# Kernel tuning notes

Hardware: AMD Instinct MI355X
Metric: run time of the kernel (lower is better)

The kernel has to match this reference:

```python
import jax, jax.numpy as jnp
import numpy as np

EMBED = 1024
HEADS = 16
HEAD_DIM = EMBED // HEADS
OUT_DIM = 1024


def setup_inputs() -> dict:
    key = jax.random.key(0)
    ks = jax.random.split(key, 8)
    N, L = 2, 2048
    values = jax.random.normal(ks[0], (N, L, EMBED), dtype=jnp.float32)
    keys_t = jax.random.normal(ks[1], (N, L, EMBED), dtype=jnp.float32)
    query = jax.random.normal(ks[2], (N, L, EMBED), dtype=jnp.float32)
    s = 1.0 / np.sqrt(HEAD_DIM)
    Wv = jax.random.normal(ks[3], (HEAD_DIM, HEAD_DIM), dtype=jnp.float32) * s
    Wk = jax.random.normal(ks[4], (HEAD_DIM, HEAD_DIM), dtype=jnp.float32) * s
    Wq = jax.random.normal(ks[5], (HEAD_DIM, HEAD_DIM), dtype=jnp.float32) * s
    Wout = jax.random.normal(ks[6], (OUT_DIM, EMBED), dtype=jnp.float32) * (1.0 / np.sqrt(EMBED))
    bout = jax.random.normal(ks[7], (OUT_DIM,), dtype=jnp.float32) * 0.01
    return {"values": values, "keys": keys_t, "query": query,
            "Wv": Wv, "Wk": Wk, "Wq": Wq, "Wout": Wout, "bout": bout}


def reference(values, keys, query, Wv, Wk, Wq, Wout, bout):
    N, Lq, _ = query.shape
    Lk = keys.shape[1]
    # split into heads: (N, L, H, D)
    v = values.reshape(N, Lk, HEADS, HEAD_DIM)
    k = keys.reshape(N, Lk, HEADS, HEAD_DIM)
    q = query.reshape(N, Lq, HEADS, HEAD_DIM)
    # per-head shared linear projections (torch Linear: x @ W.T, no bias)
    v = jnp.einsum('nlhd,ed->nlhe', v, Wv)
    k = jnp.einsum('nlhd,ed->nlhe', k, Wk)
    q = jnp.einsum('nqhd,ed->nqhe', q, Wq)
    # scores (N, H, Q, K); NOTE: scale is 1/sqrt(embed_size), per original code
    scores = jnp.einsum('nqhd,nkhd->nhqk', q, k) / jnp.sqrt(jnp.float32(EMBED))
    attn = jax.nn.softmax(scores, axis=-1)
    out = jnp.einsum('nhqk,nkhd->nqhd', attn, v).reshape(N, Lq, EMBED)
    # fc_out: x @ Wout.T + bout
    return out @ Wout.T + bout
```

## Files before the change

kernel.cpp:

```cpp
#include <hip/hip_runtime.h>
#include <cstdint>

typedef __attribute__((ext_vector_type(8))) short short8;
typedef __attribute__((ext_vector_type(4))) float floatx4;
typedef __attribute__((ext_vector_type(4))) _Float16 half4;

#define DEV __device__ __forceinline__

constexpr int NB = 2, Lseq = 2048, NH = 16, HD = 64, EMB = 1024;
constexpr float QSCALE = 0.03125f * 1.4426950408889634f;

DEV uint16_t f2bf(float f) {
  uint32_t x = __builtin_bit_cast(uint32_t, f);
  x += 0x7fffu + ((x >> 16) & 1u);
  return (uint16_t)(x >> 16);
}

DEV uint32_t pack2(float lo, float hi) {
  uint32_t a = __builtin_bit_cast(uint32_t, lo) + 0x8000u;
  uint32_t b = __builtin_bit_cast(uint32_t, hi) + 0x8000u;
  return __builtin_amdgcn_perm(b, a, 0x07060302);
}

DEV uint32_t packh2(float lo, float hi) {
  return __builtin_bit_cast(uint32_t, __builtin_amdgcn_cvt_pkrtz(lo, hi));
}

DEV void gl_lds16(const void* g, void* l) {
  __builtin_amdgcn_global_load_lds((const __attribute__((address_space(1))) void*)g,
                                   (__attribute__((address_space(3))) void*)l, 16, 0, 0);
}

DEV short8 ld8bf(const float* p, float sc) {
  float4 u = *(const float4*)p;
  float4 v = *(const float4*)(p + 4);
  union { short8 s; uint32_t d[4]; } r;
  r.d[0] = pack2(u.x * sc, u.y * sc);
  r.d[1] = pack2(u.z * sc, u.w * sc);
  r.d[2] = pack2(v.x * sc, v.y * sc);
  r.d[3] = pack2(v.z * sc, v.w * sc);
  return r.s;
}

__global__ __launch_bounds__(256) void prep_kernel(
    const float* __restrict__ values, const float* __restrict__ keysrc,
    const float* __restrict__ query, const float* __restrict__ Wv,
    const float* __restrict__ Wk, const float* __restrict__ Wq,
    const float* __restrict__ Wout,
    uint16_t* __restrict__ qp, uint16_t* __restrict__ kp,
    uint16_t* __restrict__ vp, uint16_t* __restrict__ wbf) {
  const int t = threadIdx.x, w = t >> 6, lane = t & 63;
  const int quad = lane >> 4, l16 = lane & 15;
  const int wid = blockIdx.x * 4 + w;
  const int mat = wid >> 10, sub = wid & 1023;

  if (mat == 3) {
#pragma unroll
    for (int i = 0; i < 4; ++i) {
      int idx = sub * 256 + i * 64 + lane;
      float4 v = ((const float4*)Wout)[idx];
      uint2 p;
      p.x = pack2(v.x, v.y);
      p.y = pack2(v.z, v.w);
      ((uint2*)wbf)[idx] = p;
    }
    return;
  }

  floatx4 c[4][4];
#pragma unroll
  for (int i = 0; i < 4; ++i)
#pragma unroll
    for (int j = 0; j < 4; ++j) c[i][j] = floatx4{0.f, 0.f, 0.f, 0.f};

  if (mat < 2) {
    const float* src = mat ? keysrc : query;
    const float* W   = mat ? Wk : Wq;
    const float asc  = mat ? 1.f : QSCALE;
    uint16_t* dst    = mat ? kp : qp;
    const int R0 = sub * 64;
    short8 a[4][2], b[4][2];
#pragma unroll
    for (int dc = 0; dc < 2; ++dc) {
#pragma unroll
      for (int f = 0; f < 4; ++f) {
        a[f][dc] = ld8bf(W + (size_t)(f * 16 + l16) * 64 + dc * 32 + quad * 8, asc);
        b[f][dc] = ld8bf(src + (size_t)(R0 + f * 16 + l16) * 64 + dc * 32 + quad * 8, 1.f);
      }
    }
#pragma unroll
    for (int dc = 0; dc < 2; ++dc)
#pragma unroll
      for (int mf = 0; mf < 4; ++mf)
#pragma unroll
        for (int nf = 0; nf < 4; ++nf)
          c[mf][nf] = __builtin_amdgcn_mfma_f32_16x16x32_bf16(a[mf][dc], b[nf][dc], c[mf][nf], 0, 0, 0);
#pragma unroll
    for (int nf = 0; nf < 4; ++nf) {
      int r = R0 + nf * 16 + l16;
      int h = r & 15, l = (r >> 4) & 2047, n = r >> 15;
      uint16_t* drow = dst + ((size_t)(n * 16 + h) * 2048 + l) * 64;
#pragma unroll
      for (int mf = 0; mf < 4; ++mf) {
        uint2 pk;
        pk.x = pack2(c[mf][nf][0], c[mf][nf][1]);
        pk.y = pack2(c[mf][nf][2], c[mf][nf][3]);
        *(uint2*)(drow + mf * 16 + quad * 4) = pk;
      }
    }
  } else {
    const int nh = sub >> 5, L0 = (sub & 31) * 64;
    const int n = nh >> 4, h = nh & 15;
    short8 a[4][2], b[4][2];
#pragma unroll
    for (int dc = 0; dc < 2; ++dc) {
#pragma unroll
      for (int f = 0; f < 4; ++f) {
        a[f][dc] = ld8bf(values + (size_t)(n * 2048 + L0 + f * 16 + l16) * 1024 + h * 64 + dc * 32 + quad * 8, 1.f);
        b[f][dc] = ld8bf(Wv + (size_t)(f * 16 + l16) * 64 + dc * 32 + quad * 8, 1.f);
      }
    }
#pragma unroll
    for (int dc = 0; dc < 2; ++dc)
#pragma unroll
      for (int mf = 0; mf < 4; ++mf)
#pragma unroll
        for (int nf = 0; nf < 4; ++nf)
          c[mf][nf] = __builtin_amdgcn_mfma_f32_16x16x32_bf16(a[mf][dc], b[nf][dc], c[mf][nf], 0, 0, 0);
#pragma unroll
    for (int nf = 0; nf < 4; ++nf) {
      int d = nf * 16 + l16;
      uint16_t* drow = vp + ((size_t)nh * 64 + d) * 2048 + L0;
#pragma unroll
      for (int mf = 0; mf < 4; ++mf) {
        uint2 pk;
        pk.x = packh2(c[mf][nf][0], c[mf][nf][1]);
        pk.y = packh2(c[mf][nf][2], c[mf][nf][3]);
        *(uint2*)(drow + mf * 16 + quad * 4) = pk;
      }
    }
  }
}

__global__ __launch_bounds__(256, 4) void flash_kernel(const uint16_t* __restrict__ qp,
                                                       const uint16_t* __restrict__ kp,
                                                       const uint16_t* __restrict__ vp,
                                                       float* __restrict__ opart,
                                                       float* __restrict__ psum_g) {
  constexpr int kbn = 16;
  __shared__ uint16_t Kt[2][64 * 64];
  __shared__ uint16_t Vt[2][64 * 64];
  const int t = threadIdx.x;
  const int w = t >> 6, lane = t & 63, quad = lane >> 4, l16 = lane & 15;
  const int nh = blockIdx.x, qt = blockIdx.y, kh = blockIdx.z;
  const int q0 = qt * 128 + w * 32;
  const uint16_t* Qb = qp + (size_t)nh * Lseq * HD;
  const uint16_t* Kb = kp + (size_t)nh * Lseq * HD + (size_t)kh * kbn * 64 * 64;
  const uint16_t* Vb = vp + (size_t)nh * HD * Lseq;
  const int vcol0 = kh * kbn * 64;
  const int srow = lane >> 3, sc8 = (lane & 7) ^ (lane >> 3);

  short8 bq[2][2];
#pragma unroll
  for (int qb = 0; qb < 2; ++qb) {
    bq[qb][0] = *(const short8*)(Qb + (q0 + qb * 16 + l16) * 64 + quad * 8);
    bq[qb][1] = *(const short8*)(Qb + (q0 + qb * 16 + l16) * 64 + 32 + quad * 8);
  }

  floatx4 o[4][2];
  floatx4 lfr[2];
#pragma unroll
  for (int i = 0; i < 4; ++i)
#pragma unroll
    for (int qb = 0; qb < 2; ++qb) o[i][qb] = floatx4{0.f, 0.f, 0.f, 0.f};
  lfr[0] = lfr[1] = floatx4{0.f, 0.f, 0.f, 0.f};
  const _Float16 one = (_Float16)1.0f;
  const half4 vone = {one, one, one, one};

#pragma unroll
  for (int i = 0; i < 2; ++i) {
    int r0 = w * 16 + i * 8;
    gl_lds16(Kb + (r0 + srow) * 64 + sc8 * 8, &Kt[0][r0 * 64]);
    gl_lds16(Vb + (size_t)(r0 + srow) * Lseq + vcol0 + sc8 * 8, &Vt[0][r0 * 64]);
  }

  for (int kb = 0; kb < kbn; ++kb) {
    __syncthreads();
    const int cur = kb & 1;
    if (kb + 1 < kbn) {
      const int nxt = cur ^ 1;
      const uint16_t* kg = Kb + (kb + 1) * (64 * 64);
#pragma unroll
      for (int i = 0; i < 2; ++i) {
        int r0 = w * 16 + i * 8;
        gl_lds16(kg + (r0 + srow) * 64 + sc8 * 8, &Kt[nxt][r0 * 64]);
        gl_lds16(Vb + (size_t)(r0 + srow) * Lseq + vcol0 + (kb + 1) * 64 + sc8 * 8, &Vt[nxt][r0 * 64]);
      }
    }

    floatx4 s[4][2];
#pragma unroll
    for (int kb16 = 0; kb16 < 4; ++kb16)
#pragma unroll
      for (int qb = 0; qb < 2; ++qb) s[kb16][qb] = floatx4{0.f, 0.f, 0.f, 0.f};
#pragma unroll
    for (int dc = 0; dc < 2; ++dc) {
#pragma unroll
      for (int kb16 = 0; kb16 < 4; ++kb16) {
        int row = kb16 * 16 + l16;
        short8 ak = *(const short8*)(&Kt[cur][row * 64 + ((dc * 4 + quad) ^ (row & 7)) * 8]);
        s[kb16][0] = __builtin_amdgcn_mfma_f32_16x16x32_bf16(ak, bq[0][dc], s[kb16][0], 0, 0, 0);
        s[kb16][1] = __builtin_amdgcn_mfma_f32_16x16x32_bf16(ak, bq[1][dc], s[kb16][1], 0, 0, 0);
      }
    }

    half4 bp[4][2];
#pragma unroll
    for (int qb = 0; qb < 2; ++qb) {
#pragma unroll
      for (int kb16 = 0; kb16 < 4; ++kb16) {
        float p0 = __builtin_amdgcn_exp2f(s[kb16][qb][0]);
        float p1 = __builtin_amdgcn_exp2f(s[kb16][qb][1]);
        float p2 = __builtin_amdgcn_exp2f(s[kb16][qb][2]);
        float p3 = __builtin_amdgcn_exp2f(s[kb16][qb][3]);
        union { half4 h4; uint32_t d[2]; } u;
        u.d[0] = packh2(p0, p1);
        u.d[1] = packh2(p2, p3);
        bp[kb16][qb] = u.h4;
      }
    }
#pragma unroll
    for (int kb16 = 0; kb16 < 4; ++kb16) {
      lfr[0] = __builtin_amdgcn_mfma_f32_16x16x16f16(vone, bp[kb16][0], lfr[0], 0, 0, 0);
      lfr[1] = __builtin_amdgcn_mfma_f32_16x16x16f16(vone, bp[kb16][1], lfr[1], 0, 0, 0);
    }

#pragma unroll
    for (int kb16 = 0; kb16 < 4; ++kb16) {
#pragma unroll
      for (int db = 0; db < 4; ++db) {
        int row = db * 16 + l16;
        int ch = (kb16 * 2 + (quad >> 1)) ^ (row & 7);
        half4 av = *(const half4*)(&Vt[cur][row * 64 + ch * 8 + (quad & 1) * 4]);
        o[db][0] = __builtin_amdgcn_mfma_f32_16x16x16f16(av, bp[kb16][0], o[db][0], 0, 0, 0);
        o[db][1] = __builtin_amdgcn_mfma_f32_16x16x16f16(av, bp[kb16][1], o[db][1], 0, 0, 0);
      }
    }
  }

  float* ob = opart + (((size_t)nh * 16 + qt) * 2 + kh) * 8192 + (size_t)w * 8 * 256;
#pragma unroll
  for (int db = 0; db < 4; ++db)
#pragma unroll
    for (int qb = 0; qb < 2; ++qb)
      *(floatx4*)(ob + (db * 2 + qb) * 256 + lane * 4) = o[db][qb];
  if (quad == 0) {
#pragma unroll
    for (int qb = 0; qb < 2; ++qb)
      psum_g[(((size_t)nh * 16 + qt) * 2 + kh) * 128 + w * 32 + qb * 16 + l16] = lfr[qb][0];
  }
}

__global__ __launch_bounds__(256, 2) void gemm_fused64(const float* __restrict__ opart,
                                                       const float* __restrict__ psum_g,
                                                       const uint16_t* __restrict__ Wb,
                                                       const float* __restrict__ bias,
                                                       float* __restrict__ out) {
  __shared__ uint16_t Xt[64 * 64];
  __shared__ uint16_t Wt[2][128 * 64];
  const int t = threadIdx.x, w = t >> 6, lane = t & 63, quad = lane >> 4, l16 = lane & 15;
  const int mblk = blockIdx.x, obk = blockIdx.y;
  const int n = mblk >> 5, qt = (mblk >> 1) & 15, h2 = mblk & 1;
  const int m0 = mblk * 64, o0 = obk * 128;
  const int w_orig = 2 * h2 + (w >> 1), qb = w & 1;
  const int srow = lane >> 3, sc8 = (lane & 7) ^ (lane >> 3);

  floatx4 acc[8];
#pragma unroll
  for (int j = 0; j < 8; ++j) acc[j] = floatx4{0.f, 0.f, 0.f, 0.f};

  floatx4 fa[4], fb[4];
  float la, lb;

  auto issue_loads = [&](int h) {
    size_t tb = ((size_t)(n * 16 + h) * 16 + qt) * 2;
    const float* pa = opart + tb * 8192 + (size_t)w_orig * 2048 + lane * 4;
#pragma unroll
    for (int db = 0; db < 4; ++db) {
      fa[db] = *(const floatx4*)(pa + (db * 2 + qb) * 256);
      fb[db] = *(const floatx4*)(pa + 8192 + (db * 2 + qb) * 256);
    }
    la = psum_g[tb * 128 + w_orig * 32 + qb * 16 + l16];
    lb = psum_g[tb * 128 + 128 + w_orig * 32 + qb * 16 + l16];
  };

  auto pack_write = [&]() {
    float inv = __builtin_amdgcn_rcpf(la + lb);
    int q = w * 16 + l16;
#pragma unroll
    for (int db = 0; db < 4; ++db) {
      float v0 = (fa[db][0] + fb[db][0]) * inv;
      float v1 = (fa[db][1] + fb[db][1]) * inv;
      float v2 = (fa[db][2] + fb[db][2]) * inv;
      float v3 = (fa[db][3] + fb[db][3]) * inv;
      int ch = (db * 2 + (quad >> 1)) ^ (q & 7);
      uint2 pk;
      pk.x = pack2(v0, v1);
      pk.y = pack2(v2, v3);
      *(uint2*)(&Xt[q * 64 + ch * 8 + (quad & 1) * 4]) = pk;
    }
  };

  auto dma_w = [&](int buf, int kt) {
#pragma unroll
    for (int i = 0; i < 4; ++i) {
      int r0 = w * 32 + i * 8;
      gl_lds16(Wb + (size_t)(o0 + r0 + srow) * 1024 + kt * 64 + sc8 * 8, &Wt[buf][r0 * 64]);
    }
  };

  issue_loads(0);
  pack_write();
  dma_w(0, 0);

  for (int kt = 0; kt < 16; ++kt) {
    const int cur = kt & 1;
    __syncthreads();
    if (kt + 1 < 16) {
      issue_loads(kt + 1);
      dma_w(cur ^ 1, kt + 1);
    }
#pragma unroll
    for (int kc = 0; kc < 2; ++kc) {
      int ra = w * 16 + l16;
      short8 a = *(const short8*)(&Xt[ra * 64 + ((kc * 4 + quad) ^ (ra & 7)) * 8]);
#pragma unroll
      for (int nf = 0; nf < 8; ++nf) {
        int rb = nf * 16 + l16;
        short8 b = *(const short8*)(&Wt[cur][rb * 64 + ((kc * 4 + quad) ^ (rb & 7)) * 8]);
        acc[nf] = __builtin_amdgcn_mfma_f32_16x16x32_bf16(a, b, acc[nf], 0, 0, 0);
      }
    }
    if (kt + 1 < 16) pack_write();
  }

#pragma unroll
  for (int nf = 0; nf < 8; ++nf) {
    float bv = bias[o0 + nf * 16 + l16];
#pragma unroll
    for (int r = 0; r < 4; ++r)
      out[(size_t)(m0 + w * 16 + quad * 4 + r) * 1024 + o0 + nf * 16 + l16] = acc[nf][r] + bv;
  }
}

extern "C" void kernel_launch(void* const* d_in, const int* in_sizes, int n_in,
                              void* d_out, int out_size, void* d_ws, size_t ws_size,
                              hipStream_t stream) {
  const float* values = (const float*)d_in[0];
  const float* keys   = (const float*)d_in[1];
  const float* query  = (const float*)d_in[2];
  const float* Wv     = (const float*)d_in[3];
  const float* Wk     = (const float*)d_in[4];
  const float* Wq     = (const float*)d_in[5];
  const float* Wout   = (const float*)d_in[6];
  const float* bout   = (const float*)d_in[7];
  float* out = (float*)d_out;
  (void)ws_size;

  uint16_t* ws  = (uint16_t*)d_ws;
  uint16_t* qp  = ws;
  uint16_t* kp  = ws + (size_t)4194304;
  uint16_t* vp  = ws + (size_t)8388608;
  uint16_t* wbf = ws + (size_t)12582912;
  float* opart  = (float*)(ws + (size_t)13631488);
  float* psum   = opart + (size_t)8388608;

  prep_kernel<<<dim3(1024), dim3(256), 0, stream>>>(values, keys, query, Wv, Wk, Wq, Wout,
                                                    qp, kp, vp, wbf);
  flash_kernel<<<dim3(32, 16, 2), dim3(256), 0, stream>>>(qp, kp, vp, opart, psum);
  gemm_fused64<<<dim3(64, 8), dim3(256), 0, stream>>>(opart, psum, wbf, bout, out);
}
```

Baseline: 178.3 us.

## Drop split-K in flash attention and normalize output in-kernel as bf16

```diff
diff --git a/kernel.cpp b/kernel.cpp
--- a/kernel.cpp
+++ b/kernel.cpp
@@ -145,19 +145,17 @@
 __global__ __launch_bounds__(256, 4) void flash_kernel(const uint16_t* __restrict__ qp,
                                                        const uint16_t* __restrict__ kp,
                                                        const uint16_t* __restrict__ vp,
-                                                       float* __restrict__ opart,
-                                                       float* __restrict__ psum_g) {
-  constexpr int kbn = 16;
+                                                       uint16_t* __restrict__ xg) {
+  constexpr int kbn = 32;
   __shared__ uint16_t Kt[2][64 * 64];
   __shared__ uint16_t Vt[2][64 * 64];
   const int t = threadIdx.x;
   const int w = t >> 6, lane = t & 63, quad = lane >> 4, l16 = lane & 15;
-  const int nh = blockIdx.x, qt = blockIdx.y, kh = blockIdx.z;
+  const int nh = blockIdx.x, qt = blockIdx.y;
   const int q0 = qt * 128 + w * 32;
   const uint16_t* Qb = qp + (size_t)nh * Lseq * HD;
-  const uint16_t* Kb = kp + (size_t)nh * Lseq * HD + (size_t)kh * kbn * 64 * 64;
+  const uint16_t* Kb = kp + (size_t)nh * Lseq * HD;
   const uint16_t* Vb = vp + (size_t)nh * HD * Lseq;
-  const int vcol0 = kh * kbn * 64;
   const int srow = lane >> 3, sc8 = (lane & 7) ^ (lane >> 3);
 
   short8 bq[2][2];
@@ -181,7 +179,7 @@
   for (int i = 0; i < 2; ++i) {
     int r0 = w * 16 + i * 8;
     gl_lds16(Kb + (r0 + srow) * 64 + sc8 * 8, &Kt[0][r0 * 64]);
-    gl_lds16(Vb + (size_t)(r0 + srow) * Lseq + vcol0 + sc8 * 8, &Vt[0][r0 * 64]);
+    gl_lds16(Vb + (size_t)(r0 + srow) * Lseq + sc8 * 8, &Vt[0][r0 * 64]);
   }
 
   for (int kb = 0; kb < kbn; ++kb) {
@@ -194,7 +192,7 @@
       for (int i = 0; i < 2; ++i) {
         int r0 = w * 16 + i * 8;
         gl_lds16(kg + (r0 + srow) * 64 + sc8 * 8, &Kt[nxt][r0 * 64]);
-        gl_lds16(Vb + (size_t)(r0 + srow) * Lseq + vcol0 + (kb + 1) * 64 + sc8 * 8, &Vt[nxt][r0 * 64]);
+        gl_lds16(Vb + (size_t)(r0 + srow) * Lseq + (kb + 1) * 64 + sc8 * 8, &Vt[nxt][r0 * 64]);
       }
     }
 
@@ -248,70 +246,43 @@
     }
   }
 
-  float* ob = opart + (((size_t)nh * 16 + qt) * 2 + kh) * 8192 + (size_t)w * 8 * 256;
-#pragma unroll
-  for (int db = 0; db < 4; ++db)
-#pragma unroll
-    for (int qb = 0; qb < 2; ++qb)
-      *(floatx4*)(ob + (db * 2 + qb) * 256 + lane * 4) = o[db][qb];
-  if (quad == 0) {
-#pragma unroll
-    for (int qb = 0; qb < 2; ++qb)
-      psum_g[(((size_t)nh * 16 + qt) * 2 + kh) * 128 + w * 32 + qb * 16 + l16] = lfr[qb][0];
-  }
-}
-
-__global__ __launch_bounds__(256, 2) void gemm_fused64(const float* __restrict__ opart,
-                                                       const float* __restrict__ psum_g,
-                                                       const uint16_t* __restrict__ Wb,
-                                                       const float* __restrict__ bias,
-                                                       float* __restrict__ out) {
-  __shared__ uint16_t Xt[64 * 64];
+  const int nn = nh >> 4, h = nh & 15;
+  const float inv0 = __builtin_amdgcn_rcpf(lfr[0][0]);
+  const float inv1 = __builtin_amdgcn_rcpf(lfr[1][0]);
+#pragma unroll
+  for (int qb = 0; qb < 2; ++qb) {
+    const float inv = qb ? inv1 : inv0;
+    uint16_t* xr = xg + ((size_t)(nn * 2048 + q0 + qb * 16 + l16)) * 1024 + h * 64 + quad * 4;
+#pragma unroll
+    for (int db = 0; db < 4; ++db) {
+      uint2 pk;
+      pk.x = pack2(o[db][qb][0] * inv, o[db][qb][1] * inv);
+      pk.y = pack2(o[db][qb][2] * inv, o[db][qb][3] * inv);
+      *(uint2*)(xr + db * 16) = pk;
+    }
+  }
+}
+
+__global__ __launch_bounds__(256, 2) void out_gemm(const uint16_t* __restrict__ Xg,
+                                                   const uint16_t* __restrict__ Wb,
+                                                   const float* __restrict__ bias,
+                                                   float* __restrict__ out) {
+  __shared__ uint16_t Xt[2][64 * 64];
   __shared__ uint16_t Wt[2][128 * 64];
   const int t = threadIdx.x, w = t >> 6, lane = t & 63, quad = lane >> 4, l16 = lane & 15;
-  const int mblk = blockIdx.x, obk = blockIdx.y;
-  const int n = mblk >> 5, qt = (mblk >> 1) & 15, h2 = mblk & 1;
-  const int m0 = mblk * 64, o0 = obk * 128;
-  const int w_orig = 2 * h2 + (w >> 1), qb = w & 1;
+  const int m0 = blockIdx.x * 64, o0 = blockIdx.y * 128;
   const int srow = lane >> 3, sc8 = (lane & 7) ^ (lane >> 3);
 
   floatx4 acc[8];
 #pragma unroll
   for (int j = 0; j < 8; ++j) acc[j] = floatx4{0.f, 0.f, 0.f, 0.f};
 
-  floatx4 fa[4], fb[4];
-  float la, lb;
-
-  auto issue_loads = [&](int h) {
-    size_t tb = ((size_t)(n * 16 + h) * 16 + qt) * 2;
-    const float* pa = opart + tb * 8192 + (size_t)w_orig * 2048 + lane * 4;
-#pragma unroll
-    for (int db = 0; db < 4; ++db) {
-      fa[db] = *(const floatx4*)(pa + (db * 2 + qb) * 256);
-      fb[db] = *(const floatx4*)(pa + 8192 + (db * 2 + qb) * 256);
-    }
-    la = psum_g[tb * 128 + w_orig * 32 + qb * 16 + l16];
-    lb = psum_g[tb * 128 + 128 + w_orig * 32 + qb * 16 + l16];
-  };
-
-  auto pack_write = [&]() {
-    float inv = __builtin_amdgcn_rcpf(la + lb);
-    int q = w * 16 + l16;
-#pragma unroll
-    for (int db = 0; db < 4; ++db) {
-      float v0 = (fa[db][0] + fb[db][0]) * inv;
-      float v1 = (fa[db][1] + fb[db][1]) * inv;
-      float v2 = (fa[db][2] + fb[db][2]) * inv;
-      float v3 = (fa[db][3] + fb[db][3]) * inv;
-      int ch = (db * 2 + (quad >> 1)) ^ (q & 7);
-      uint2 pk;
-      pk.x = pack2(v0, v1);
-      pk.y = pack2(v2, v3);
-      *(uint2*)(&Xt[q * 64 + ch * 8 + (quad & 1) * 4]) = pk;
-    }
-  };
-
-  auto dma_w = [&](int buf, int kt) {
+  auto stage = [&](int buf, int kt) {
+#pragma unroll
+    for (int i = 0; i < 2; ++i) {
+      int r0 = w * 16 + i * 8;
+      gl_lds16(Xg + (size_t)(m0 + r0 + srow) * 1024 + kt * 64 + sc8 * 8, &Xt[buf][r0 * 64]);
+    }
 #pragma unroll
     for (int i = 0; i < 4; ++i) {
       int r0 = w * 32 + i * 8;
@@ -319,21 +290,16 @@
     }
   };
 
-  issue_loads(0);
-  pack_write();
-  dma_w(0, 0);
+  stage(0, 0);
 
   for (int kt = 0; kt < 16; ++kt) {
     const int cur = kt & 1;
     __syncthreads();
-    if (kt + 1 < 16) {
-      issue_loads(kt + 1);
-      dma_w(cur ^ 1, kt + 1);
-    }
+    if (kt + 1 < 16) stage(cur ^ 1, kt + 1);
 #pragma unroll
     for (int kc = 0; kc < 2; ++kc) {
       int ra = w * 16 + l16;
-      short8 a = *(const short8*)(&Xt[ra * 64 + ((kc * 4 + quad) ^ (ra & 7)) * 8]);
+      short8 a = *(const short8*)(&Xt[cur][ra * 64 + ((kc * 4 + quad) ^ (ra & 7)) * 8]);
 #pragma unroll
       for (int nf = 0; nf < 8; ++nf) {
         int rb = nf * 16 + l16;
@@ -341,7 +307,6 @@
         acc[nf] = __builtin_amdgcn_mfma_f32_16x16x32_bf16(a, b, acc[nf], 0, 0, 0);
       }
     }
-    if (kt + 1 < 16) pack_write();
   }
 
 #pragma unroll
@@ -372,11 +337,10 @@
   uint16_t* kp  = ws + (size_t)4194304;
   uint16_t* vp  = ws + (size_t)8388608;
   uint16_t* wbf = ws + (size_t)12582912;
-  float* opart  = (float*)(ws + (size_t)13631488);
-  float* psum   = opart + (size_t)8388608;
+  uint16_t* xp  = ws + (size_t)13631488;
 
   prep_kernel<<<dim3(1024), dim3(256), 0, stream>>>(values, keys, query, Wv, Wk, Wq, Wout,
                                                     qp, kp, vp, wbf);
-  flash_kernel<<<dim3(32, 16, 2), dim3(256), 0, stream>>>(qp, kp, vp, opart, psum);
-  gemm_fused64<<<dim3(64, 8), dim3(256), 0, stream>>>(opart, psum, wbf, bout, out);
-}
+  flash_kernel<<<dim3(32, 16), dim3(256), 0, stream>>>(qp, kp, vp, xp);
+  out_gemm<<<dim3(64, 8), dim3(256), 0, stream>>>(xp, wbf, bout, out);
+}
```

After: 182.6 us. +2.4%, slower.
